# Kernel optimization log

Hardware: AMD Instinct MI355X
Metric: run time of the kernel (lower is better)

The kernel has to match this reference:

```python
import jax, jax.numpy as jnp
import numpy as np

N_NODES = 50000
N_EDGES = 800000
D_IN, D_HID, D_ENC = 256, 128, 64


def setup_inputs() -> dict:
    key = jax.random.key(0)
    ks = jax.random.split(key, 8)
    x = jax.random.normal(ks[0], (N_NODES, D_IN), dtype=jnp.float32)
    edge_index = jax.random.randint(ks[1], (2, N_EDGES), 0, N_NODES, dtype=jnp.int64)
    # GCNConv params: lin weight (no bias) + separate bias, stored as [in, out]
    W1 = jax.random.normal(ks[2], (D_IN, D_HID), dtype=jnp.float32) * (1.0 / np.sqrt(D_IN))
    b1 = jnp.zeros((D_HID,), dtype=jnp.float32)
    W2 = jax.random.normal(ks[3], (D_HID, D_ENC), dtype=jnp.float32) * (1.0 / np.sqrt(D_HID))
    b2 = jnp.zeros((D_ENC,), dtype=jnp.float32)
    Wfc = jax.random.normal(ks[4], (D_ENC, 1), dtype=jnp.float32) * (1.0 / np.sqrt(D_ENC))
    bfc = jnp.zeros((1,), dtype=jnp.float32)
    return {"x": x, "edge_index": edge_index, "W1": W1, "b1": b1,
            "W2": W2, "b2": b2, "Wfc": Wfc, "bfc": bfc}


def gcn_conv(x, W, b, row, col, norm, n_nodes):
    """PyG GCNConv (normalize=True): D^-1/2 (A+I) D^-1/2 X W + b."""
    h = x @ W                                   # [N, out]
    msg = h[row] * norm[:, None]                # [E+N, out] gather + scale
    out = jax.ops.segment_sum(msg, col, num_segments=n_nodes)  # scatter-add
    return out + b


def gcn_norm(edge_index, n_nodes, dtype):
    loop = jnp.arange(n_nodes, dtype=edge_index.dtype)
    row = jnp.concatenate([edge_index[0], loop])  # sources
    col = jnp.concatenate([edge_index[1], loop])  # targets
    deg = jax.ops.segment_sum(jnp.ones_like(col, dtype=dtype), col,
                              num_segments=n_nodes)
    dinv = jnp.where(deg > 0, jax.lax.rsqrt(jnp.maximum(deg, 1e-12)), 0.0)
    norm = dinv[row] * dinv[col]
    return row, col, norm


def reference(x, edge_index, W1, b1, W2, b2, Wfc, bfc):
    n = x.shape[0]
    row, col, norm = gcn_norm(edge_index, n, x.dtype)
    h = gcn_conv(x, W1, b1, row, col, norm, n)
    h = jax.nn.relu(h)
    # dropout p=0 / eval mode: identity
    h = gcn_conv(h, W2, b2, row, col, norm, n)
    out = jax.nn.sigmoid(h @ Wfc + bfc)          # [N, 1]
    return out
```

## Files before the change

kernel.cpp:

```cpp
#include <hip/hip_runtime.h>
#include <hip/hip_bf16.h>
#include <cmath>

#define N_NODES 50000
#define N_EDGES 800000
#define D_IN 256
#define D_HID 128
#define D_ENC 64
#define NBUK 128
#define BSH 9
#define BMSK 511
#define BCAP 16384
#define PBF_EPT 8
#define NPARTB 196
#define NGEMB 782

typedef short short8 __attribute__((ext_vector_type(8)));
typedef float floatx4 __attribute__((ext_vector_type(4)));
typedef float floatx8 __attribute__((ext_vector_type(8)));
typedef unsigned short ushort8v __attribute__((ext_vector_type(8)));

static __device__ __forceinline__ unsigned short f2bf(float f) {
    unsigned int u = __float_as_uint(f);
    unsigned int r = (u + 0x7FFFu + ((u >> 16) & 1u)) >> 16;
    return (unsigned short)r;
}
static __device__ __forceinline__ float bf2f(unsigned short u) {
    return __uint_as_float(((unsigned int)u) << 16);
}
static __device__ __forceinline__ floatx8 bf2f8(ushort8v u) {
    floatx8 f;
#pragma unroll
    for (int j = 0; j < 8; ++j) f[j] = bf2f(u[j]);
    return f;
}

static __device__ __forceinline__ void wswz(const float* __restrict__ W,
                                            unsigned short* __restrict__ Wsw,
                                            int t, int K, int N) {
    int KS = K / 32;
    int lane = t & 63;
    int ks   = (t >> 6) % KS;
    int ct   = (t >> 6) / KS;
    int m = lane & 15, quad = lane >> 4;
    int kbase = ks * 32 + quad * 8;
    int col   = ct * 16 + m;
#pragma unroll
    for (int j = 0; j < 8; ++j)
        Wsw[t * 8 + j] = f2bf(W[(size_t)(kbase + j) * N + col]);
}

__global__ __launch_bounds__(256) void prep_k(const float* __restrict__ W1,
                                              const float* __restrict__ W2,
                                              const float* __restrict__ b2,
                                              const float* __restrict__ Wfc,
                                              unsigned short* __restrict__ Wsw1,
                                              float* __restrict__ w2fc,
                                              float* __restrict__ b2fc,
                                              int* __restrict__ bcur) {
    int t = blockIdx.x * 256 + threadIdx.x;
    if (t < 4096) wswz(W1, Wsw1, t, D_IN, D_HID);
    else if (t < 4224) {
        int c = t - 4096;
        float s = 0.0f;
#pragma unroll 8
        for (int j = 0; j < D_ENC; ++j) s += W2[c * D_ENC + j] * Wfc[j];
        w2fc[c] = s;
    } else if (t == 4224) {
        float s = 0.0f;
        for (int j = 0; j < D_ENC; ++j) s += b2[j] * Wfc[j];
        b2fc[0] = s;
    } else if (t >= 4225 && t < 4225 + NBUK) {
        bcur[t - 4225] = 0;
    }
}

__global__ __launch_bounds__(512) void partgemm_k(const int* __restrict__ rows,
                                                  const int* __restrict__ cols,
                                                  int* __restrict__ bcur,
                                                  unsigned int* __restrict__ brecs,
                                                  const float4* __restrict__ X4,
                                                  const unsigned short* __restrict__ Wsw,
                                                  unsigned short* __restrict__ H) {
    extern __shared__ char dynsm[];
    int tid = threadIdx.x;
    if (blockIdx.x < NPARTB) {
        unsigned int* recs = (unsigned int*)dynsm;
        int* h     = (int*)(dynsm + 16384);
        int* ex    = h + NBUK;
        int* gbase = ex + NBUK;
        if (tid < NBUK) h[tid] = 0;
        __syncthreads();
        int e0 = blockIdx.x * 4096;
        unsigned int myrec[PBF_EPT];
        int myb[PBF_EPT];
#pragma unroll
        for (int j = 0; j < PBF_EPT; ++j) {
            int e = e0 + j * 512 + tid;
            if (e < N_EDGES) {
                int s = rows[e], d = cols[e];
                myrec[j] = ((unsigned int)s << 16) | (unsigned int)d;
                myb[j] = d >> BSH;
                atomicAdd(&h[myb[j]], 1);
            } else myb[j] = -1;
        }
        __syncthreads();
        if (tid < NBUK) {
            int c = h[tid];
            gbase[tid] = tid * BCAP + (c ? atomicAdd(&bcur[tid], c) : 0);
            ex[tid] = c;
        }
        __syncthreads();
        for (int off = 1; off < NBUK; off <<= 1) {
            int v = 0;
            if (tid < NBUK && tid >= off) v = ex[tid - off];
            __syncthreads();
            if (tid < NBUK) ex[tid] += v;
            __syncthreads();
        }
        if (tid < NBUK) { ex[tid] -= h[tid]; h[tid] = 0; }
        __syncthreads();
#pragma unroll
        for (int j = 0; j < PBF_EPT; ++j) {
            if (myb[j] >= 0) {
                int p = ex[myb[j]] + atomicAdd(&h[myb[j]], 1);
                recs[p] = myrec[j];
            }
        }
        __syncthreads();
        int w = tid >> 6, lane = tid & 63;
        for (int b = w; b < NBUK; b += 8) {
            int start = ex[b], cnt = h[b], gb = gbase[b];
            int lim = (b + 1) * BCAP;
            for (int i = lane; i < cnt; i += 64) {
                int gp = gb + i;
                if (gp < lim) brecs[gp] = recs[start + i];
            }
        }
    } else {
        constexpr int KP = D_IN + 8;
        unsigned short* As = (unsigned short*)dynsm;
        int row0 = (blockIdx.x - NPARTB) * 64;
        for (int idx = tid; idx < 64 * 64; idx += 512) {
            int r = idx >> 6, c4 = idx & 63;
            int gr = row0 + r;
            float4 v = (gr < N_NODES) ? X4[(size_t)gr * 64 + c4] : float4{0, 0, 0, 0};
            __hip_bfloat162 p0 = __float22bfloat162_rn(float2{v.x, v.y});
            __hip_bfloat162 p1 = __float22bfloat162_rn(float2{v.z, v.w});
            uint2 u; u.x = *(unsigned int*)&p0; u.y = *(unsigned int*)&p1;
            *(uint2*)&As[r * KP + c4 * 4] = u;
        }
        __syncthreads();

        int w    = tid >> 6;
        int lane = tid & 63;
        int m    = lane & 15;
        int quad = lane >> 4;
        int rsub = w & 3;
        int cth  = w >> 2;

        floatx4 acc[4];
#pragma unroll
        for (int ct = 0; ct < 4; ++ct)
#pragma unroll
            for (int i = 0; i < 4; ++i) acc[ct][i] = 0.0f;

#pragma unroll
        for (int ks = 0; ks < D_IN / 32; ++ks) {
            short8 af = *(const short8*)&As[(rsub * 16 + m) * KP + ks * 32 + quad * 8];
#pragma unroll
            for (int ct = 0; ct < 4; ++ct) {
                int ct4 = cth * 4 + ct;
                short8 bf = *(const short8*)&Wsw[(size_t)((ct4 * (D_IN / 32) + ks) * 64 + lane) * 8];
                acc[ct] = __builtin_amdgcn_mfma_f32_16x16x32_bf16(af, bf, acc[ct], 0, 0, 0);
            }
        }

        int rbase = row0 + rsub * 16 + quad * 4;
#pragma unroll
        for (int ct = 0; ct < 4; ++ct) {
            int col = (cth * 4 + ct) * 16 + m;
#pragma unroll
            for (int reg = 0; reg < 4; ++reg) {
                int r = rbase + reg;
                if (r < N_NODES) H[(size_t)r * D_HID + col] = f2bf(acc[ct][reg]);
            }
        }
    }
}

__global__ __launch_bounds__(512) void bucket_csr_k(const unsigned int* __restrict__ brecs,
                                                    const int* __restrict__ bcur,
                                                    int* __restrict__ rowptr,
                                                    int* __restrict__ rowcnt,
                                                    unsigned short* __restrict__ srcs,
                                                    float* __restrict__ dinv) {
    __shared__ int s[512];
    __shared__ int cur[512];
    __shared__ unsigned short sl[BCAP];
    int b = blockIdx.x;
    int cb = bcur[b]; if (cb > BCAP) cb = BCAP;
    int ebeg = b * BCAP, eend = ebeg + cb;
    int tid = threadIdx.x;
    s[tid] = 0;
    __syncthreads();
    for (int e = ebeg + tid; e < eend; e += 512)
        atomicAdd(&s[brecs[e] & BMSK], 1);
    __syncthreads();
    int v = s[tid];
    for (int off = 1; off < 512; off <<= 1) {
        int t = (tid >= off) ? s[tid - off] : 0;
        __syncthreads();
        s[tid] += t;
        __syncthreads();
    }
    int excl = s[tid] - v;
    cur[tid] = excl;
    int node = (b << BSH) + tid;
    if (node < N_NODES) {
        rowptr[node] = ebeg + excl;
        rowcnt[node] = v;
        dinv[node] = rsqrtf((float)(v + 1));
    }
    __syncthreads();
    for (int e = ebeg + tid; e < eend; e += 512) {
        unsigned int rec = brecs[e];
        int p = atomicAdd(&cur[rec & BMSK], 1);
        sl[p] = (unsigned short)(rec >> 16);
    }
    __syncthreads();
    int nw = (cb + 1) >> 1;
    unsigned int* s32 = (unsigned int*)(srcs + ebeg);
    const unsigned int* l32 = (const unsigned int*)sl;
    for (int t = tid; t < nw; t += 512) s32[t] = l32[t];
}

#define WGATHER(SP)                                                            \
    {                                                                          \
        const auto* sp_ = (SP);                                                \
        int i = 0;                                                             \
        for (; i + 8 <= cnt; i += 8) {                                         \
            int s0 = sp_[i],     s1 = sp_[i + 1], s2 = sp_[i + 2], s3 = sp_[i + 3]; \
            int s4 = sp_[i + 4], s5 = sp_[i + 5], s6 = sp_[i + 6], s7 = sp_[i + 7]; \
            float w0 = dinv[s0], w1 = dinv[s1], w2 = dinv[s2], w3 = dinv[s3];  \
            float w4 = dinv[s4], w5 = dinv[s5], w6 = dinv[s6], w7 = dinv[s7];  \
            ushort8v v0 = hs[(size_t)s0 * 16 + d8], v1 = hs[(size_t)s1 * 16 + d8]; \
            ushort8v v2 = hs[(size_t)s2 * 16 + d8], v3 = hs[(size_t)s3 * 16 + d8]; \
            ushort8v v4 = hs[(size_t)s4 * 16 + d8], v5 = hs[(size_t)s5 * 16 + d8]; \
            ushort8v v6 = hs[(size_t)s6 * 16 + d8], v7 = hs[(size_t)s7 * 16 + d8]; \
            a0 += bf2f8(v0) * w0; a1 += bf2f8(v1) * w1;                        \
            a2 += bf2f8(v2) * w2; a3 += bf2f8(v3) * w3;                        \
            a0 += bf2f8(v4) * w4; a1 += bf2f8(v5) * w5;                        \
            a2 += bf2f8(v6) * w6; a3 += bf2f8(v7) * w7;                        \
        }                                                                      \
        if (i + 4 <= cnt) {                                                    \
            int s0 = sp_[i], s1 = sp_[i + 1], s2 = sp_[i + 2], s3 = sp_[i + 3]; \
            a0 += bf2f8(hs[(size_t)s0 * 16 + d8]) * dinv[s0];                  \
            a1 += bf2f8(hs[(size_t)s1 * 16 + d8]) * dinv[s1];                  \
            a2 += bf2f8(hs[(size_t)s2 * 16 + d8]) * dinv[s2];                  \
            a3 += bf2f8(hs[(size_t)s3 * 16 + d8]) * dinv[s3];                  \
            i += 4;                                                            \
        }                                                                      \
        for (; i < cnt; ++i) {                                                 \
            int s = sp_[i];                                                    \
            a0 += bf2f8(hs[(size_t)s * 16 + d8]) * dinv[s];                    \
        }                                                                      \
    }

__global__ __launch_bounds__(256) void g1z_k(const ushort8v* __restrict__ hs,
                                             const int* __restrict__ rowptr,
                                             const int* __restrict__ rowcnt,
                                             const unsigned short* __restrict__ srcs,
                                             const float* __restrict__ dinv,
                                             const float4* __restrict__ b1_4,
                                             const float4* __restrict__ w2fc4,
                                             float* __restrict__ z) {
    __shared__ unsigned short sidx[1024];
    __shared__ int sb2[2];
    int tid = threadIdx.x;
    int nodeb = blockIdx.x * 16;
    int ln = tid >> 4;
    int d8 = tid & 15;
    int node = nodeb + ln;
    int beg = rowptr[node];
    int cnt = rowcnt[node];
    if (tid == 0)   sb2[0] = beg;
    if (tid == 240) sb2[1] = beg + cnt;
    ushort8v selfv = hs[(size_t)node * 16 + d8];
    float di = dinv[node];
    __syncthreads();
    int base = sb2[0], total = sb2[1] - base;
    for (int t = tid; t < total && t < 1024; t += 256) sidx[t] = srcs[base + t];
    __syncthreads();

    floatx8 a0 = {0,0,0,0,0,0,0,0}, a1 = a0, a2 = a0, a3 = a0;
    if (total <= 1024) {
        WGATHER(sidx + (beg - base))
    } else {
        WGATHER(srcs + beg)
    }
    floatx8 acc = a0 + a1 + a2 + a3 + bf2f8(selfv) * di;
    float4 bA = b1_4[d8 * 2],  bB = b1_4[d8 * 2 + 1];
    float4 wA = w2fc4[d8 * 2], wB = w2fc4[d8 * 2 + 1];
    float s = fmaxf(di * acc[0] + bA.x, 0.0f) * wA.x
            + fmaxf(di * acc[1] + bA.y, 0.0f) * wA.y
            + fmaxf(di * acc[2] + bA.z, 0.0f) * wA.z
            + fmaxf(di * acc[3] + bA.w, 0.0f) * wA.w
            + fmaxf(di * acc[4] + bB.x, 0.0f) * wB.x
            + fmaxf(di * acc[5] + bB.y, 0.0f) * wB.y
            + fmaxf(di * acc[6] + bB.z, 0.0f) * wB.z
            + fmaxf(di * acc[7] + bB.w, 0.0f) * wB.w;
#pragma unroll
    for (int off = 8; off; off >>= 1) s += __shfl_xor(s, off, 16);
    if (d8 == 0) z[node] = di * s;
}

__global__ __launch_bounds__(256) void gatherz_k(const float* __restrict__ z,
                                                 const int* __restrict__ rowptr,
                                                 const int* __restrict__ rowcnt,
                                                 const unsigned short* __restrict__ srcs,
                                                 const float* __restrict__ dinv,
                                                 const float* __restrict__ b2fc,
                                                 const float* __restrict__ bfc,
                                                 float* __restrict__ out) {
    int v = blockIdx.x * 256 + threadIdx.x;
    if (v >= N_NODES) return;
    int beg = rowptr[v], cnt = rowcnt[v];
    float s0 = z[v], s1 = 0.0f, s2 = 0.0f, s3 = 0.0f;
    int i = beg, end = beg + cnt;
    for (; i + 4 <= end; i += 4) {
        s0 += z[srcs[i]];
        s1 += z[srcs[i + 1]];
        s2 += z[srcs[i + 2]];
        s3 += z[srcs[i + 3]];
    }
    for (; i < end; ++i) s0 += z[srcs[i]];
    float p = dinv[v] * (s0 + s1 + s2 + s3) + b2fc[0] + bfc[0];
    out[v] = 1.0f / (1.0f + expf(-p));
}

extern "C" void kernel_launch(void* const* d_in, const int* in_sizes, int n_in,
                              void* d_out, int out_size, void* d_ws, size_t ws_size,
                              hipStream_t stream) {
    const float* x   = (const float*)d_in[0];
    const int*   ei  = (const int*)d_in[1];
    const float* W1  = (const float*)d_in[2];
    const float* b1  = (const float*)d_in[3];
    const float* W2  = (const float*)d_in[4];
    const float* b2  = (const float*)d_in[5];
    const float* Wfc = (const float*)d_in[6];
    const float* bfc = (const float*)d_in[7];
    float* out = (float*)d_out;

    const int* rows = ei;
    const int* cols = ei + N_EDGES;

    float* ws     = (float*)d_ws;
    float* dinv   = ws;
    int*   rowptr = (int*)(ws + 50048);
    int*   rowcnt = rowptr + 50048;
    int*   bcur   = rowcnt + 50048;
    unsigned int* brecs = (unsigned int*)(bcur + 128);
    unsigned short* srcs = (unsigned short*)(brecs + NBUK * BCAP);
    unsigned short* h1 = srcs + (size_t)NBUK * BCAP;
    unsigned short* Wsw1 = h1 + (size_t)N_NODES * D_HID;
    float* z    = (float*)(Wsw1 + (size_t)D_IN * D_HID);
    float* w2fc = z + 50000;
    float* b2fc = w2fc + 128;

    prep_k<<<18, 256, 0, stream>>>(W1, W2, b2, Wfc, Wsw1, w2fc, b2fc, bcur);

    partgemm_k<<<NPARTB + NGEMB, 512, 36864, stream>>>(rows, cols, bcur, brecs,
                                                       (const float4*)x, Wsw1, h1);

    bucket_csr_k<<<(N_NODES + 511) / 512, 512, 0, stream>>>(brecs, bcur, rowptr, rowcnt, srcs, dinv);

    g1z_k<<<N_NODES / 16, 256, 0, stream>>>((const ushort8v*)h1, rowptr, rowcnt, srcs, dinv,
                                            (const float4*)b1, (const float4*)w2fc, z);

    gatherz_k<<<(N_NODES + 255) / 256, 256, 0, stream>>>(z, rowptr, rowcnt, srcs, dinv,
                                                         b2fc, bfc, out);
}
```

Baseline: 161.2 us.

## Fuse CSR build and second gather into prior kernels via atomic-counter block dependencies

Result: slower. 400.8 us (+148.7%).

```diff
diff --git a/kernel.cpp b/kernel.cpp
--- a/kernel.cpp
+++ b/kernel.cpp
@@ -14,6 +14,9 @@
 #define PBF_EPT 8
 #define NPARTB 196
 #define NGEMB 782
+#define NCSRB 98
+#define NG1ZB 3125
+#define NGZB  196
 
 typedef short short8 __attribute__((ext_vector_type(8)));
 typedef float floatx4 __attribute__((ext_vector_type(4)));
@@ -33,6 +36,19 @@
 #pragma unroll
     for (int j = 0; j < 8; ++j) f[j] = bf2f(u[j]);
     return f;
+}
+
+static __device__ __forceinline__ void block_release(int* ctr) {
+    __syncthreads();
+    if (threadIdx.x == 0) { __threadfence(); atomicAdd(ctr, 1); }
+}
+static __device__ __forceinline__ void block_acquire(int* ctr, int n) {
+    if (threadIdx.x == 0) {
+        while (__hip_atomic_load(ctr, __ATOMIC_RELAXED, __HIP_MEMORY_SCOPE_AGENT) < n)
+            __builtin_amdgcn_s_sleep(8);
+        __threadfence();
+    }
+    __syncthreads();
 }
 
 static __device__ __forceinline__ void wswz(const float* __restrict__ W,
@@ -57,7 +73,8 @@
                                               unsigned short* __restrict__ Wsw1,
                                               float* __restrict__ w2fc,
                                               float* __restrict__ b2fc,
-                                              int* __restrict__ bcur) {
+                                              int* __restrict__ bcur,
+                                              int* __restrict__ ctrs) {
     int t = blockIdx.x * 256 + threadIdx.x;
     if (t < 4096) wswz(W1, Wsw1, t, D_IN, D_HID);
     else if (t < 4224) {
@@ -72,16 +89,23 @@
         b2fc[0] = s;
     } else if (t >= 4225 && t < 4225 + NBUK) {
         bcur[t - 4225] = 0;
-    }
-}
-
-__global__ __launch_bounds__(512) void partgemm_k(const int* __restrict__ rows,
-                                                  const int* __restrict__ cols,
-                                                  int* __restrict__ bcur,
-                                                  unsigned int* __restrict__ brecs,
-                                                  const float4* __restrict__ X4,
-                                                  const unsigned short* __restrict__ Wsw,
-                                                  unsigned short* __restrict__ H) {
+    } else if (t == 4225 + NBUK || t == 4226 + NBUK) {
+        ctrs[t - 4225 - NBUK] = 0;
+    }
+}
+
+__global__ __launch_bounds__(512) void fused_k(const int* __restrict__ rows,
+                                               const int* __restrict__ cols,
+                                               int* __restrict__ bcur,
+                                               unsigned int* __restrict__ brecs,
+                                               const float4* __restrict__ X4,
+                                               const unsigned short* __restrict__ Wsw,
+                                               unsigned short* __restrict__ H,
+                                               int* __restrict__ rowptr,
+                                               int* __restrict__ rowcnt,
+                                               unsigned short* __restrict__ srcs,
+                                               float* __restrict__ dinv,
+                                               int* __restrict__ ctr0) {
     extern __shared__ char dynsm[];
     int tid = threadIdx.x;
     if (blockIdx.x < NPARTB) {
@@ -137,7 +161,8 @@
                 if (gp < lim) brecs[gp] = recs[start + i];
             }
         }
-    } else {
+        block_release(ctr0);
+    } else if (blockIdx.x < NPARTB + NGEMB) {
         constexpr int KP = D_IN + 8;
         unsigned short* As = (unsigned short*)dynsm;
         int row0 = (blockIdx.x - NPARTB) * 64;
@@ -186,53 +211,46 @@
                 if (r < N_NODES) H[(size_t)r * D_HID + col] = f2bf(acc[ct][reg]);
             }
         }
-    }
-}
-
-__global__ __launch_bounds__(512) void bucket_csr_k(const unsigned int* __restrict__ brecs,
-                                                    const int* __restrict__ bcur,
-                                                    int* __restrict__ rowptr,
-                                                    int* __restrict__ rowcnt,
-                                                    unsigned short* __restrict__ srcs,
-                                                    float* __restrict__ dinv) {
-    __shared__ int s[512];
-    __shared__ int cur[512];
-    __shared__ unsigned short sl[BCAP];
-    int b = blockIdx.x;
-    int cb = bcur[b]; if (cb > BCAP) cb = BCAP;
-    int ebeg = b * BCAP, eend = ebeg + cb;
-    int tid = threadIdx.x;
-    s[tid] = 0;
-    __syncthreads();
-    for (int e = ebeg + tid; e < eend; e += 512)
-        atomicAdd(&s[brecs[e] & BMSK], 1);
-    __syncthreads();
-    int v = s[tid];
-    for (int off = 1; off < 512; off <<= 1) {
-        int t = (tid >= off) ? s[tid - off] : 0;
-        __syncthreads();
-        s[tid] += t;
-        __syncthreads();
-    }
-    int excl = s[tid] - v;
-    cur[tid] = excl;
-    int node = (b << BSH) + tid;
-    if (node < N_NODES) {
-        rowptr[node] = ebeg + excl;
-        rowcnt[node] = v;
-        dinv[node] = rsqrtf((float)(v + 1));
-    }
-    __syncthreads();
-    for (int e = ebeg + tid; e < eend; e += 512) {
-        unsigned int rec = brecs[e];
-        int p = atomicAdd(&cur[rec & BMSK], 1);
-        sl[p] = (unsigned short)(rec >> 16);
-    }
-    __syncthreads();
-    int nw = (cb + 1) >> 1;
-    unsigned int* s32 = (unsigned int*)(srcs + ebeg);
-    const unsigned int* l32 = (const unsigned int*)sl;
-    for (int t = tid; t < nw; t += 512) s32[t] = l32[t];
+    } else {
+        block_acquire(ctr0, NPARTB);
+        int* s   = (int*)dynsm;
+        int* cur = (int*)(dynsm + 2048);
+        unsigned short* sl = (unsigned short*)(dynsm + 4096);
+        int b = blockIdx.x - NPARTB - NGEMB;
+        int cb = bcur[b]; if (cb > BCAP) cb = BCAP;
+        int ebeg = b * BCAP, eend = ebeg + cb;
+        s[tid] = 0;
+        __syncthreads();
+        for (int e = ebeg + tid; e < eend; e += 512)
+            atomicAdd(&s[brecs[e] & BMSK], 1);
+        __syncthreads();
+        int v = s[tid];
+        for (int off = 1; off < 512; off <<= 1) {
+            int t = (tid >= off) ? s[tid - off] : 0;
+            __syncthreads();
+            s[tid] += t;
+            __syncthreads();
+        }
+        int excl = s[tid] - v;
+        cur[tid] = excl;
+        int node = (b << BSH) + tid;
+        if (node < N_NODES) {
+            rowptr[node] = ebeg + excl;
+            rowcnt[node] = v;
+            dinv[node] = rsqrtf((float)(v + 1));
+        }
+        __syncthreads();
+        for (int e = ebeg + tid; e < eend; e += 512) {
+            unsigned int rec = brecs[e];
+            int p = atomicAdd(&cur[rec & BMSK], 1);
+            sl[p] = (unsigned short)(rec >> 16);
+        }
+        __syncthreads();
+        int nw = (cb + 1) >> 1;
+        unsigned int* s32 = (unsigned int*)(srcs + ebeg);
+        const unsigned int* l32 = (const unsigned int*)sl;
+        for (int t = tid; t < nw; t += 512) s32[t] = l32[t];
+    }
 }
 
 #define WGATHER(SP)                                                            \
@@ -267,76 +285,75 @@
         }                                                                      \
     }
 
-__global__ __launch_bounds__(256) void g1z_k(const ushort8v* __restrict__ hs,
-                                             const int* __restrict__ rowptr,
-                                             const int* __restrict__ rowcnt,
-                                             const unsigned short* __restrict__ srcs,
-                                             const float* __restrict__ dinv,
-                                             const float4* __restrict__ b1_4,
-                                             const float4* __restrict__ w2fc4,
-                                             float* __restrict__ z) {
+__global__ __launch_bounds__(256) void g1zz_k(const ushort8v* __restrict__ hs,
+                                              const int* __restrict__ rowptr,
+                                              const int* __restrict__ rowcnt,
+                                              const unsigned short* __restrict__ srcs,
+                                              const float* __restrict__ dinv,
+                                              const float4* __restrict__ b1_4,
+                                              const float4* __restrict__ w2fc4,
+                                              float* __restrict__ z,
+                                              int* __restrict__ ctr1,
+                                              const float* __restrict__ b2fc,
+                                              const float* __restrict__ bfc,
+                                              float* __restrict__ out) {
     __shared__ unsigned short sidx[1024];
     __shared__ int sb2[2];
     int tid = threadIdx.x;
-    int nodeb = blockIdx.x * 16;
-    int ln = tid >> 4;
-    int d8 = tid & 15;
-    int node = nodeb + ln;
-    int beg = rowptr[node];
-    int cnt = rowcnt[node];
-    if (tid == 0)   sb2[0] = beg;
-    if (tid == 240) sb2[1] = beg + cnt;
-    ushort8v selfv = hs[(size_t)node * 16 + d8];
-    float di = dinv[node];
-    __syncthreads();
-    int base = sb2[0], total = sb2[1] - base;
-    for (int t = tid; t < total && t < 1024; t += 256) sidx[t] = srcs[base + t];
-    __syncthreads();
-
-    floatx8 a0 = {0,0,0,0,0,0,0,0}, a1 = a0, a2 = a0, a3 = a0;
-    if (total <= 1024) {
-        WGATHER(sidx + (beg - base))
+    if (blockIdx.x < NG1ZB) {
+        int nodeb = blockIdx.x * 16;
+        int ln = tid >> 4;
+        int d8 = tid & 15;
+        int node = nodeb + ln;
+        int beg = rowptr[node];
+        int cnt = rowcnt[node];
+        if (tid == 0)   sb2[0] = beg;
+        if (tid == 240) sb2[1] = beg + cnt;
+        ushort8v selfv = hs[(size_t)node * 16 + d8];
+        float di = dinv[node];
+        __syncthreads();
+        int base = sb2[0], total = sb2[1] - base;
+        for (int t = tid; t < total && t < 1024; t += 256) sidx[t] = srcs[base + t];
+        __syncthreads();
+
+        floatx8 a0 = {0,0,0,0,0,0,0,0}, a1 = a0, a2 = a0, a3 = a0;
+        if (total <= 1024) {
+            WGATHER(sidx + (beg - base))
+        } else {
+            WGATHER(srcs + beg)
+        }
+        floatx8 acc = a0 + a1 + a2 + a3 + bf2f8(selfv) * di;
+        float4 bA = b1_4[d8 * 2],  bB = b1_4[d8 * 2 + 1];
+        float4 wA = w2fc4[d8 * 2], wB = w2fc4[d8 * 2 + 1];
+        float s = fmaxf(di * acc[0] + bA.x, 0.0f) * wA.x
+                + fmaxf(di * acc[1] + bA.y, 0.0f) * wA.y
+                + fmaxf(di * acc[2] + bA.z, 0.0f) * wA.z
+                + fmaxf(di * acc[3] + bA.w, 0.0f) * wA.w
+                + fmaxf(di * acc[4] + bB.x, 0.0f) * wB.x
+                + fmaxf(di * acc[5] + bB.y, 0.0f) * wB.y
+                + fmaxf(di * acc[6] + bB.z, 0.0f) * wB.z
+                + fmaxf(di * acc[7] + bB.w, 0.0f) * wB.w;
+#pragma unroll
+        for (int off = 8; off; off >>= 1) s += __shfl_xor(s, off, 16);
+        if (d8 == 0) z[node] = di * s;
+        block_release(ctr1);
     } else {
-        WGATHER(srcs + beg)
-    }
-    floatx8 acc = a0 + a1 + a2 + a3 + bf2f8(selfv) * di;
-    float4 bA = b1_4[d8 * 2],  bB = b1_4[d8 * 2 + 1];
-    float4 wA = w2fc4[d8 * 2], wB = w2fc4[d8 * 2 + 1];
-    float s = fmaxf(di * acc[0] + bA.x, 0.0f) * wA.x
-            + fmaxf(di * acc[1] + bA.y, 0.0f) * wA.y
-            + fmaxf(di * acc[2] + bA.z, 0.0f) * wA.z
-            + fmaxf(di * acc[3] + bA.w, 0.0f) * wA.w
-            + fmaxf(di * acc[4] + bB.x, 0.0f) * wB.x
-            + fmaxf(di * acc[5] + bB.y, 0.0f) * wB.y
-            + fmaxf(di * acc[6] + bB.z, 0.0f) * wB.z
-            + fmaxf(di * acc[7] + bB.w, 0.0f) * wB.w;
-#pragma unroll
-    for (int off = 8; off; off >>= 1) s += __shfl_xor(s, off, 16);
-    if (d8 == 0) z[node] = di * s;
-}
-
-__global__ __launch_bounds__(256) void gatherz_k(const float* __restrict__ z,
-                                                 const int* __restrict__ rowptr,
-                                                 const int* __restrict__ rowcnt,
-                                                 const unsigned short* __restrict__ srcs,
-                                                 const float* __restrict__ dinv,
-                                                 const float* __restrict__ b2fc,
-                                                 const float* __restrict__ bfc,
-                                                 float* __restrict__ out) {
-    int v = blockIdx.x * 256 + threadIdx.x;
-    if (v >= N_NODES) return;
-    int beg = rowptr[v], cnt = rowcnt[v];
-    float s0 = z[v], s1 = 0.0f, s2 = 0.0f, s3 = 0.0f;
-    int i = beg, end = beg + cnt;
-    for (; i + 4 <= end; i += 4) {
-        s0 += z[srcs[i]];
-        s1 += z[srcs[i + 1]];
-        s2 += z[srcs[i + 2]];
-        s3 += z[srcs[i + 3]];
-    }
-    for (; i < end; ++i) s0 += z[srcs[i]];
-    float p = dinv[v] * (s0 + s1 + s2 + s3) + b2fc[0] + bfc[0];
-    out[v] = 1.0f / (1.0f + expf(-p));
+        block_acquire(ctr1, NG1ZB);
+        int v = (blockIdx.x - NG1ZB) * 256 + tid;
+        if (v >= N_NODES) return;
+        int beg = rowptr[v], cnt = rowcnt[v];
+        float s0 = z[v], s1 = 0.0f, s2 = 0.0f, s3 = 0.0f;
+        int i = beg, end = beg + cnt;
+        for (; i + 4 <= end; i += 4) {
+            s0 += z[srcs[i]];
+            s1 += z[srcs[i + 1]];
+            s2 += z[srcs[i + 2]];
+            s3 += z[srcs[i + 3]];
+        }
+        for (; i < end; ++i) s0 += z[srcs[i]];
+        float p = dinv[v] * (s0 + s1 + s2 + s3) + b2fc[0] + bfc[0];
+        out[v] = 1.0f / (1.0f + expf(-p));
+    }
 }
 
 extern "C" void kernel_launch(void* const* d_in, const int* in_sizes, int n_in,
@@ -367,17 +384,15 @@
     float* z    = (float*)(Wsw1 + (size_t)D_IN * D_HID);
     float* w2fc = z + 50000;
     float* b2fc = w2fc + 128;
-
-    prep_k<<<18, 256, 0, stream>>>(W1, W2, b2, Wfc, Wsw1, w2fc, b2fc, bcur);
-
-    partgemm_k<<<NPARTB + NGEMB, 512, 36864, stream>>>(rows, cols, bcur, brecs,
-                                                       (const float4*)x, Wsw1, h1);
-
-    bucket_csr_k<<<(N_NODES + 511) / 512, 512, 0, stream>>>(brecs, bcur, rowptr, rowcnt, srcs, dinv);
-
-    g1z_k<<<N_NODES / 16, 256, 0, stream>>>((const ushort8v*)h1, rowptr, rowcnt, srcs, dinv,
-                                            (const float4*)b1, (const float4*)w2fc, z);
-
-    gatherz_k<<<(N_NODES + 255) / 256, 256, 0, stream>>>(z, rowptr, rowcnt, srcs, dinv,
-                                                         b2fc, bfc, out);
-}
+    int*   ctrs = (int*)(b2fc + 1);
+
+    prep_k<<<18, 256, 0, stream>>>(W1, W2, b2, Wfc, Wsw1, w2fc, b2fc, bcur, ctrs);
+
+    fused_k<<<NPARTB + NGEMB + NCSRB, 512, 36864, stream>>>(
+        rows, cols, bcur, brecs, (const float4*)x, Wsw1, h1,
+        rowptr, rowcnt, srcs, dinv, ctrs);
+
+    g1zz_k<<<NG1ZB + NGZB, 256, 0, stream>>>((const ushort8v*)h1, rowptr, rowcnt, srcs, dinv,
+                                             (const float4*)b1, (const float4*)w2fc, z,
+                                             ctrs + 1, b2fc, bfc, out);
+}
```

## Split GEMM across partition and CSR kernels to overlap with bucket build

Applied to the files above, without the earlier changes.

Result: no change. 162.7 us (+1.0%).

```diff
diff --git a/kernel.cpp b/kernel.cpp
--- a/kernel.cpp
+++ b/kernel.cpp
@@ -14,6 +14,9 @@
 #define PBF_EPT 8
 #define NPARTB 196
 #define NGEMB 782
+#define NGEMB_H 391
+#define GEMM_H2_ROW0 (NGEMB_H * 64)
+#define NCSRB 98
 
 typedef short short8 __attribute__((ext_vector_type(8)));
 typedef float floatx4 __attribute__((ext_vector_type(4)));
@@ -75,133 +78,80 @@
     }
 }
 
-__global__ __launch_bounds__(512) void partgemm_k(const int* __restrict__ rows,
-                                                  const int* __restrict__ cols,
-                                                  int* __restrict__ bcur,
-                                                  unsigned int* __restrict__ brecs,
-                                                  const float4* __restrict__ X4,
-                                                  const unsigned short* __restrict__ Wsw,
-                                                  unsigned short* __restrict__ H) {
-    extern __shared__ char dynsm[];
+static __device__ void part_path(char* dynsm, int bid,
+                                 const int* __restrict__ rows,
+                                 const int* __restrict__ cols,
+                                 int* __restrict__ bcur,
+                                 unsigned int* __restrict__ brecs) {
+    unsigned int* recs = (unsigned int*)dynsm;
+    int* h     = (int*)(dynsm + 16384);
+    int* ex    = h + NBUK;
+    int* gbase = ex + NBUK;
     int tid = threadIdx.x;
-    if (blockIdx.x < NPARTB) {
-        unsigned int* recs = (unsigned int*)dynsm;
-        int* h     = (int*)(dynsm + 16384);
-        int* ex    = h + NBUK;
-        int* gbase = ex + NBUK;
-        if (tid < NBUK) h[tid] = 0;
+    if (tid < NBUK) h[tid] = 0;
+    __syncthreads();
+    int e0 = bid * 4096;
+    unsigned int myrec[PBF_EPT];
+    int myb[PBF_EPT];
+#pragma unroll
+    for (int j = 0; j < PBF_EPT; ++j) {
+        int e = e0 + j * 512 + tid;
+        if (e < N_EDGES) {
+            int s = __builtin_nontemporal_load(&rows[e]);
+            int d = __builtin_nontemporal_load(&cols[e]);
+            myrec[j] = ((unsigned int)s << 16) | (unsigned int)d;
+            myb[j] = d >> BSH;
+            atomicAdd(&h[myb[j]], 1);
+        } else myb[j] = -1;
+    }
+    __syncthreads();
+    if (tid < NBUK) {
+        int c = h[tid];
+        gbase[tid] = tid * BCAP + (c ? atomicAdd(&bcur[tid], c) : 0);
+        ex[tid] = c;
+    }
+    __syncthreads();
+    for (int off = 1; off < NBUK; off <<= 1) {
+        int v = 0;
+        if (tid < NBUK && tid >= off) v = ex[tid - off];
         __syncthreads();
-        int e0 = blockIdx.x * 4096;
-        unsigned int myrec[PBF_EPT];
-        int myb[PBF_EPT];
-#pragma unroll
-        for (int j = 0; j < PBF_EPT; ++j) {
-            int e = e0 + j * 512 + tid;
-            if (e < N_EDGES) {
-                int s = rows[e], d = cols[e];
-                myrec[j] = ((unsigned int)s << 16) | (unsigned int)d;
-                myb[j] = d >> BSH;
-                atomicAdd(&h[myb[j]], 1);
-            } else myb[j] = -1;
+        if (tid < NBUK) ex[tid] += v;
+        __syncthreads();
+    }
+    if (tid < NBUK) { ex[tid] -= h[tid]; h[tid] = 0; }
+    __syncthreads();
+#pragma unroll
+    for (int j = 0; j < PBF_EPT; ++j) {
+        if (myb[j] >= 0) {
+            int p = ex[myb[j]] + atomicAdd(&h[myb[j]], 1);
+            recs[p] = myrec[j];
         }
-        __syncthreads();
-        if (tid < NBUK) {
-            int c = h[tid];
-            gbase[tid] = tid * BCAP + (c ? atomicAdd(&bcur[tid], c) : 0);
-            ex[tid] = c;
+    }
+    __syncthreads();
+    int w = tid >> 6, lane = tid & 63;
+    for (int b = w; b < NBUK; b += 8) {
+        int start = ex[b], cnt = h[b], gb = gbase[b];
+        int lim = (b + 1) * BCAP;
+        for (int i = lane; i < cnt; i += 64) {
+            int gp = gb + i;
+            if (gp < lim) brecs[gp] = recs[start + i];
         }
-        __syncthreads();
-        for (int off = 1; off < NBUK; off <<= 1) {
-            int v = 0;
-            if (tid < NBUK && tid >= off) v = ex[tid - off];
-            __syncthreads();
-            if (tid < NBUK) ex[tid] += v;
-            __syncthreads();
-        }
-        if (tid < NBUK) { ex[tid] -= h[tid]; h[tid] = 0; }
-        __syncthreads();
-#pragma unroll
-        for (int j = 0; j < PBF_EPT; ++j) {
-            if (myb[j] >= 0) {
-                int p = ex[myb[j]] + atomicAdd(&h[myb[j]], 1);
-                recs[p] = myrec[j];
-            }
-        }
-        __syncthreads();
-        int w = tid >> 6, lane = tid & 63;
-        for (int b = w; b < NBUK; b += 8) {
-            int start = ex[b], cnt = h[b], gb = gbase[b];
-            int lim = (b + 1) * BCAP;
-            for (int i = lane; i < cnt; i += 64) {
-                int gp = gb + i;
-                if (gp < lim) brecs[gp] = recs[start + i];
-            }
-        }
-    } else {
-        constexpr int KP = D_IN + 8;
-        unsigned short* As = (unsigned short*)dynsm;
-        int row0 = (blockIdx.x - NPARTB) * 64;
-        for (int idx = tid; idx < 64 * 64; idx += 512) {
-            int r = idx >> 6, c4 = idx & 63;
-            int gr = row0 + r;
-            float4 v = (gr < N_NODES) ? X4[(size_t)gr * 64 + c4] : float4{0, 0, 0, 0};
-            __hip_bfloat162 p0 = __float22bfloat162_rn(float2{v.x, v.y});
-            __hip_bfloat162 p1 = __float22bfloat162_rn(float2{v.z, v.w});
-            uint2 u; u.x = *(unsigned int*)&p0; u.y = *(unsigned int*)&p1;
-            *(uint2*)&As[r * KP + c4 * 4] = u;
-        }
-        __syncthreads();
-
-        int w    = tid >> 6;
-        int lane = tid & 63;
-        int m    = lane & 15;
-        int quad = lane >> 4;
-        int rsub = w & 3;
-        int cth  = w >> 2;
-
-        floatx4 acc[4];
-#pragma unroll
-        for (int ct = 0; ct < 4; ++ct)
-#pragma unroll
-            for (int i = 0; i < 4; ++i) acc[ct][i] = 0.0f;
-
-#pragma unroll
-        for (int ks = 0; ks < D_IN / 32; ++ks) {
-            short8 af = *(const short8*)&As[(rsub * 16 + m) * KP + ks * 32 + quad * 8];
-#pragma unroll
-            for (int ct = 0; ct < 4; ++ct) {
-                int ct4 = cth * 4 + ct;
-                short8 bf = *(const short8*)&Wsw[(size_t)((ct4 * (D_IN / 32) + ks) * 64 + lane) * 8];
-                acc[ct] = __builtin_amdgcn_mfma_f32_16x16x32_bf16(af, bf, acc[ct], 0, 0, 0);
-            }
-        }
-
-        int rbase = row0 + rsub * 16 + quad * 4;
-#pragma unroll
-        for (int ct = 0; ct < 4; ++ct) {
-            int col = (cth * 4 + ct) * 16 + m;
-#pragma unroll
-            for (int reg = 0; reg < 4; ++reg) {
-                int r = rbase + reg;
-                if (r < N_NODES) H[(size_t)r * D_HID + col] = f2bf(acc[ct][reg]);
-            }
-        }
-    }
-}
-
-__global__ __launch_bounds__(512) void bucket_csr_k(const unsigned int* __restrict__ brecs,
-                                                    const int* __restrict__ bcur,
-                                                    int* __restrict__ rowptr,
-                                                    int* __restrict__ rowcnt,
-                                                    unsigned short* __restrict__ srcs,
-                                                    float* __restrict__ dinv) {
-    __shared__ int s[512];
-    __shared__ int cur[512];
-    __shared__ unsigned short sl[BCAP];
-    int b = blockIdx.x;
+    }
+}
+
+static __device__ void csr_path(char* dynsm, int b,
+                                const unsigned int* __restrict__ brecs,
+                                const int* __restrict__ bcur,
+                                int* __restrict__ rowptr,
+                                int* __restrict__ rowcnt,
+                                unsigned short* __restrict__ srcs,
+                                float* __restrict__ dinv) {
+    int* s   = (int*)dynsm;
+    int* cur = (int*)(dynsm + 2048);
+    unsigned short* sl = (unsigned short*)(dynsm + 4096);
+    int tid = threadIdx.x;
     int cb = bcur[b]; if (cb > BCAP) cb = BCAP;
     int ebeg = b * BCAP, eend = ebeg + cb;
-    int tid = threadIdx.x;
     s[tid] = 0;
     __syncthreads();
     for (int e = ebeg + tid; e < eend; e += 512)
@@ -233,6 +183,91 @@
     unsigned int* s32 = (unsigned int*)(srcs + ebeg);
     const unsigned int* l32 = (const unsigned int*)sl;
     for (int t = tid; t < nw; t += 512) s32[t] = l32[t];
+}
+
+static __device__ void gemm_path(char* dynsm, int row0,
+                                 const floatx4* __restrict__ X4,
+                                 const unsigned short* __restrict__ Wsw,
+                                 unsigned short* __restrict__ H) {
+    constexpr int KP = D_IN + 8;
+    unsigned short* As = (unsigned short*)dynsm;
+    int tid = threadIdx.x;
+    for (int idx = tid; idx < 64 * 64; idx += 512) {
+        int r = idx >> 6, c4 = idx & 63;
+        int gr = row0 + r;
+        floatx4 v = (gr < N_NODES) ? __builtin_nontemporal_load(&X4[(size_t)gr * 64 + c4])
+                                   : (floatx4){0, 0, 0, 0};
+        __hip_bfloat162 p0 = __float22bfloat162_rn(float2{v[0], v[1]});
+        __hip_bfloat162 p1 = __float22bfloat162_rn(float2{v[2], v[3]});
+        uint2 u; u.x = *(unsigned int*)&p0; u.y = *(unsigned int*)&p1;
+        *(uint2*)&As[r * KP + c4 * 4] = u;
+    }
+    __syncthreads();
+
+    int w    = tid >> 6;
+    int lane = tid & 63;
+    int m    = lane & 15;
+    int quad = lane >> 4;
+    int rsub = w & 3;
+    int cth  = w >> 2;
+
+    floatx4 acc[4];
+#pragma unroll
+    for (int ct = 0; ct < 4; ++ct)
+#pragma unroll
+        for (int i = 0; i < 4; ++i) acc[ct][i] = 0.0f;
+
+#pragma unroll
+    for (int ks = 0; ks < D_IN / 32; ++ks) {
+        short8 af = *(const short8*)&As[(rsub * 16 + m) * KP + ks * 32 + quad * 8];
+#pragma unroll
+        for (int ct = 0; ct < 4; ++ct) {
+            int ct4 = cth * 4 + ct;
+            short8 bf = *(const short8*)&Wsw[(size_t)((ct4 * (D_IN / 32) + ks) * 64 + lane) * 8];
+            acc[ct] = __builtin_amdgcn_mfma_f32_16x16x32_bf16(af, bf, acc[ct], 0, 0, 0);
+        }
+    }
+
+    int rbase = row0 + rsub * 16 + quad * 4;
+#pragma unroll
+    for (int ct = 0; ct < 4; ++ct) {
+        int col = (cth * 4 + ct) * 16 + m;
+#pragma unroll
+        for (int reg = 0; reg < 4; ++reg) {
+            int r = rbase + reg;
+            if (r < N_NODES) H[(size_t)r * D_HID + col] = f2bf(acc[ct][reg]);
+        }
+    }
+}
+
+__global__ __launch_bounds__(512) void pg1_k(const int* __restrict__ rows,
+                                             const int* __restrict__ cols,
+                                             int* __restrict__ bcur,
+                                             unsigned int* __restrict__ brecs,
+                                             const floatx4* __restrict__ X4,
+                                             const unsigned short* __restrict__ Wsw,
+                                             unsigned short* __restrict__ H) {
+    extern __shared__ char dynsm[];
+    if (blockIdx.x < NPARTB)
+        part_path(dynsm, blockIdx.x, rows, cols, bcur, brecs);
+    else
+        gemm_path(dynsm, (blockIdx.x - NPARTB) * 64, X4, Wsw, H);
+}
+
+__global__ __launch_bounds__(512) void cg2_k(const unsigned int* __restrict__ brecs,
+                                             const int* __restrict__ bcur,
+                                             int* __restrict__ rowptr,
+                                             int* __restrict__ rowcnt,
+                                             unsigned short* __restrict__ srcs,
+                                             float* __restrict__ dinv,
+                                             const floatx4* __restrict__ X4,
+                                             const unsigned short* __restrict__ Wsw,
+                                             unsigned short* __restrict__ H) {
+    extern __shared__ char dynsm[];
+    if (blockIdx.x < NCSRB)
+        csr_path(dynsm, blockIdx.x, brecs, bcur, rowptr, rowcnt, srcs, dinv);
+    else
+        gemm_path(dynsm, (blockIdx.x - NCSRB) * 64 + GEMM_H2_ROW0, X4, Wsw, H);
 }
 
 #define WGATHER(SP)                                                            \
@@ -370,10 +405,11 @@
 
     prep_k<<<18, 256, 0, stream>>>(W1, W2, b2, Wfc, Wsw1, w2fc, b2fc, bcur);
 
-    partgemm_k<<<NPARTB + NGEMB, 512, 36864, stream>>>(rows, cols, bcur, brecs,
-                                                       (const float4*)x, Wsw1, h1);
-
-    bucket_csr_k<<<(N_NODES + 511) / 512, 512, 0, stream>>>(brecs, bcur, rowptr, rowcnt, srcs, dinv);
+    pg1_k<<<NPARTB + NGEMB_H, 512, 36864, stream>>>(rows, cols, bcur, brecs,
+                                                    (const floatx4*)x, Wsw1, h1);
+
+    cg2_k<<<NCSRB + NGEMB_H, 512, 36864, stream>>>(brecs, bcur, rowptr, rowcnt, srcs, dinv,
+                                                   (const floatx4*)x, Wsw1, h1);
 
     g1z_k<<<N_NODES / 16, 256, 0, stream>>>((const ushort8v*)h1, rowptr, rowcnt, srcs, dinv,
                                             (const float4*)b1, (const float4*)w2fc, z);
```
